# Kernel tuning notes

Hardware: AMD Instinct MI355X
Metric: run time of the kernel (lower is better)

The kernel has to match this reference:

```python
import jax, jax.numpy as jnp
import numpy as np


def setup_inputs() -> dict:
    key = jax.random.key(0)
    k1, k2, k3, k4 = jax.random.split(key, 4)
    T, B, D_in, D_out = 512, 128, 512, 512
    X = jax.random.normal(k1, (T, B, D_in), dtype=jnp.float32)
    # torch nn.Linear default init: U(-1/sqrt(fan_in), 1/sqrt(fan_in))
    lim_in = 1.0 / np.sqrt(D_in)
    lim_h = 1.0 / np.sqrt(D_out)
    W_in = jax.random.uniform(k2, (D_out, D_in), jnp.float32, -lim_in, lim_in)
    W_h = jax.random.uniform(k3, (D_out, D_out), jnp.float32, -lim_h, lim_h)
    b_h = jax.random.uniform(k4, (D_out,), jnp.float32, -lim_h, lim_h)
    return {"X": X, "W_in": W_in, "W_h": W_h, "b_h": b_h}


def reference(X, W_in, W_h, b_h):
    # X: [T, B, D_in]. h_{t+1} = sigmoid(x_t @ W_in^T + h_t @ W_h^T + b_h)
    B = X.shape[1]
    D_out = W_h.shape[0]
    # Precompute all input projections in one big GEMM (same math).
    Xproj = jnp.einsum('tbi,oi->tbo', X, W_in)  # [T, B, D_out]
    h0 = jnp.zeros((B, D_out), dtype=X.dtype)

    def step(h, xp):
        h_new = jax.nn.sigmoid(xp + h @ W_h.T + b_h)
        return h_new, None

    h_last, _ = jax.lax.scan(step, h0, Xproj)
    return h_last
```

## Files before the change

kernel.cpp:

```cpp
#include <hip/hip_runtime.h>
#include <hip/hip_bf16.h>
#include <stdint.h>

typedef _Float16 f16;
typedef _Float16 f16x2 __attribute__((ext_vector_type(2)));
typedef _Float16 f16x4 __attribute__((ext_vector_type(4)));
typedef _Float16 f16x8 __attribute__((ext_vector_type(8)));
typedef float f32x4 __attribute__((ext_vector_type(4)));
typedef int   i32x4 __attribute__((ext_vector_type(4)));

#define T_STEPS 512
#define BATCH   128
#define DD      512
#define LOG2E   1.44269504088896f

#define XP_OFF  0
#define WF_OFF  (67108864)
#define WHQ_OFF (67108864 + 524288)
#define SC_OFF  (67108864 + 524288 + 262144)

__device__ __forceinline__ f16x2 pk(float a, float b) {
    return __builtin_bit_cast(f16x2, __builtin_amdgcn_cvt_pkrtz(a, b));
}

__device__ __forceinline__ float fast_exp2(float x) {
#if __has_builtin(__builtin_amdgcn_exp2f)
    return __builtin_amdgcn_exp2f(x);
#else
    return exp2f(x);
#endif
}

__device__ __forceinline__ float fast_rcp(float x) {
#if __has_builtin(__builtin_amdgcn_rcpf)
    return __builtin_amdgcn_rcpf(x);
#else
    return 1.0f / x;
#endif
}

__device__ __forceinline__ uint32_t pack_u8(float s, int pos, uint32_t old) {
#if __has_builtin(__builtin_amdgcn_cvt_pk_u8_f32)
    return __builtin_amdgcn_cvt_pk_u8_f32(s, pos, old);
#else
    return old | (((uint32_t)(int)s & 0xFF) << (8 * pos));
#endif
}

#define GLDS(g, l) __builtin_amdgcn_global_load_lds(                               \
        (const __attribute__((address_space(1))) void*)(g),                        \
        (__attribute__((address_space(3))) void*)(l), 16, 0, 0)

__global__ __launch_bounds__(256) void prep_kernel(
        const float* __restrict__ Win, f16* __restrict__ Wf) {
    int idx = blockIdx.x * 256 + threadIdx.x;
    if (idx < 262144) Wf[idx] = (f16)Win[idx];
}

__global__ __launch_bounds__(64) void quant_kernel(
        const float* __restrict__ Wh, char* __restrict__ Whq, float* __restrict__ scales) {
    const int o = blockIdx.x, t = threadIdx.x;
    const float* row = Wh + (size_t)o * 512;
    float v[8];
    float m = 0.f;
#pragma unroll
    for (int j = 0; j < 8; j++) { v[j] = row[t * 8 + j]; m = fmaxf(m, fabsf(v[j])); }
#pragma unroll
    for (int off = 32; off > 0; off >>= 1) m = fmaxf(m, __shfl_xor(m, off));
    if (t == 0) scales[o] = -LOG2E * m * (1.0f / (127.0f * 127.0f));
    const float inv = 127.0f / m;
    const int rt = o >> 4, rl = o & 15;
    const int k0 = t * 8;
    const int ks = k0 >> 6, qq = (k0 >> 4) & 3, j0 = k0 & 15;
    const int l = qq * 16 + rl;
    char* dst = Whq + ((size_t)((rt * 8 + ks) * 64 + l)) * 16 + j0;
#pragma unroll
    for (int j = 0; j < 8; j++) dst[j] = (char)rintf(v[j] * inv);
}

__global__ __launch_bounds__(512, 2) void gemm_kernel(
        const float* __restrict__ X, const f16* __restrict__ Wf,
        const float* __restrict__ bias, f16* __restrict__ Xp) {
    const int tid = threadIdx.x;
    const int l = tid & 63, w = tid >> 6;
    const int q = l >> 4, rl = l & 15;
    const int wm = w >> 2, wn = w & 3;
    const int blk = blockIdx.x;
    const int xcd = blk & 7, idx = blk >> 3;
    const int m_blk = (xcd * 64 + (idx >> 1)) * 128;
    const int n_blk = (idx & 1) * 256;

    __shared__ __align__(16) float As[3][128 * 32];
    __shared__ __align__(16) f16   Bs[3][256 * 32];

    const float* aSrc[2];
#pragma unroll
    for (int c = 0; c < 2; c++)
        aSrc[c] = X + (size_t)(m_blk + w * 16 + c * 8 + (l >> 3)) * 512
                    + (((l & 7) ^ (l >> 3)) << 2);
    const f16* bSrc[2];
#pragma unroll
    for (int c = 0; c < 2; c++)
        bSrc[c] = Wf + (size_t)(n_blk + c * 128 + w * 16 + (l >> 2)) * 512
                     + (((l & 3) ^ ((l >> 3) & 3)) << 3);

#define STAGE(kt, sel) do {                                                        \
        const int kf_ = (kt) * 32;                                                 \
        GLDS(aSrc[0] + kf_, &As[sel][(w * 16 + 0) * 32]);                          \
        GLDS(aSrc[1] + kf_, &As[sel][(w * 16 + 8) * 32]);                          \
        GLDS(bSrc[0] + kf_, &Bs[sel][(0 * 128 + w * 16) * 32]);                    \
        GLDS(bSrc[1] + kf_, &Bs[sel][(1 * 128 + w * 16) * 32]);                    \
    } while (0)

    f32x4 acc[4][4] = {};
    const int swA0 = (((2 * q)     ^ (rl & 7)) << 2);
    const int swA1 = (((2 * q + 1) ^ (rl & 7)) << 2);
    const int swB  = ((q ^ ((rl >> 1) & 3)) << 3);

    STAGE(0, 0);
    STAGE(1, 1);

#pragma unroll
    for (int t = 0; t < 16; ++t) {
        const int cur = t % 3;
        if (t < 15) asm volatile("s_waitcnt vmcnt(4)" ::: "memory");
        else        asm volatile("s_waitcnt vmcnt(0)" ::: "memory");
        __builtin_amdgcn_s_barrier();
        if (t + 2 < 16) STAGE(t + 2, (t + 2) % 3);

        f16x8 af4[4], bf4[4];
#pragma unroll
        for (int i = 0; i < 4; i++) {
            const int row = wm * 64 + i * 16 + rl;
            const float4 h0 = *(const float4*)&As[cur][row * 32 + swA0];
            const float4 h1 = *(const float4*)&As[cur][row * 32 + swA1];
            f16x2 p0 = pk(h0.x, h0.y), p1 = pk(h0.z, h0.w);
            f16x2 p2 = pk(h1.x, h1.y), p3 = pk(h1.z, h1.w);
            f16x8 tv;
            tv[0] = p0[0]; tv[1] = p0[1]; tv[2] = p1[0]; tv[3] = p1[1];
            tv[4] = p2[0]; tv[5] = p2[1]; tv[6] = p3[0]; tv[7] = p3[1];
            af4[i] = tv;
        }
#pragma unroll
        for (int j = 0; j < 4; j++) {
            const int row = wn * 64 + j * 16 + rl;
            bf4[j] = *(const f16x8*)&Bs[cur][row * 32 + swB];
        }
#pragma unroll
        for (int i = 0; i < 4; i++)
#pragma unroll
            for (int j = 0; j < 4; j++)
                acc[i][j] = __builtin_amdgcn_mfma_f32_16x16x32_f16(bf4[j], af4[i], acc[i][j], 0, 0, 0);
    }
#undef STAGE
#pragma unroll
    for (int j = 0; j < 4; j++) {
        const float4 b4 = *(const float4*)&bias[n_blk + wn * 64 + j * 16 + q * 4];
        const float bb[4] = {b4.x, b4.y, b4.z, b4.w};
#pragma unroll
        for (int i = 0; i < 4; i++) {
            const int m = m_blk + wm * 64 + i * 16 + rl;
            f16x4 v;
#pragma unroll
            for (int r = 0; r < 4; r++)
                v[r] = (f16)(-LOG2E * (acc[i][j][r] + bb[r]));
            *(f16x4*)(Xp + (size_t)m * 512 + n_blk + wn * 64 + j * 16 + q * 4) = v;
        }
    }
}

__global__ __launch_bounds__(1024) void rnn_kernel(
        const char* __restrict__ Whq, const float* __restrict__ scales,
        const f16* __restrict__ Xp, float* __restrict__ out) {
    const int wg = blockIdx.x;
    const int tid = threadIdx.x;
    const int l = tid & 63, w = tid >> 6;
    const int bl = l & 15;
    const int q = l >> 4;
    const int b = wg * 16 + bl;

    __shared__ __align__(16) uint32_t hT[2][2048];

    i32x4 af[2][8];
    {
        const i32x4* wp = (const i32x4*)Whq;
#pragma unroll
        for (int mt = 0; mt < 2; mt++)
#pragma unroll
            for (int ks = 0; ks < 8; ks++)
                af[mt][ks] = wp[((w * 2 + mt) * 8 + ks) * 64 + l];
    }
    float sc[2][4];
#pragma unroll
    for (int mt = 0; mt < 2; mt++)
#pragma unroll
        for (int r = 0; r < 4; r++)
            sc[mt][r] = scales[w * 32 + mt * 16 + q * 4 + r];

    for (int i = tid; i < 2048; i += 1024) hT[0][i] = 0u;
    __syncthreads();

    const f16* xpb = Xp + (size_t)b * 512 + w * 32 + q * 4;
    f16x4 xn0 = *(const f16x4*)(xpb);
    f16x4 xn1 = *(const f16x4*)(xpb + 16);

    const float K127 = 1.0f / 127.0f;
    for (int t = 0; t < T_STEPS; t++) {
        f16x4 xc0 = xn0, xc1 = xn1;
        const size_t tn = (size_t)(t < T_STEPS - 1 ? t + 1 : t) * (BATCH * 512);
        xn0 = *(const f16x4*)(xpb + tn);
        xn1 = *(const f16x4*)(xpb + tn + 16);

        const int rb = t & 1;
        i32x4 acc[2] = {};
        const uint32_t* hrow = &hT[rb][l * 4];
#pragma unroll
        for (int ks = 0; ks < 8; ks++) {
            i32x4 bfr = *(const i32x4*)(hrow + ks * 256);
            acc[0] = __builtin_amdgcn_mfma_i32_16x16x64_i8(af[0][ks], bfr, acc[0], 0, 0, 0);
            acc[1] = __builtin_amdgcn_mfma_i32_16x16x64_i8(af[1][ks], bfr, acc[1], 0, 0, 0);
        }
#pragma unroll
        for (int mt = 0; mt < 2; mt++) {
            uint32_t pkq = 0;
#pragma unroll
            for (int r = 0; r < 4; r++) {
                float tt = fmaf((float)acc[mt][r], sc[mt][r], (float)(mt == 0 ? xc0[r] : xc1[r]));
                float e  = fast_exp2(tt);
                float eq = fmaf(e, K127, K127);
                float sg = fast_rcp(eq) + 0.5f;
                pkq = pack_u8(sg, r, pkq);
            }
            hT[1 - rb][(w * 2 + mt) * 64 + bl * 4 + q] = pkq;
        }
        __syncthreads();
    }
#pragma unroll
    for (int mt = 0; mt < 2; mt++) {
        uint32_t pkq = hT[T_STEPS & 1][(w * 2 + mt) * 64 + bl * 4 + q];
        float4 o;
        o.x = (float)((pkq      ) & 0xFF) * K127;
        o.y = (float)((pkq >>  8) & 0xFF) * K127;
        o.z = (float)((pkq >> 16) & 0xFF) * K127;
        o.w = (float)((pkq >> 24) & 0xFF) * K127;
        *(float4*)(out + (size_t)b * 512 + w * 32 + mt * 16 + q * 4) = o;
    }
}

extern "C" void kernel_launch(void* const* d_in, const int* in_sizes, int n_in,
                              void* d_out, int out_size, void* d_ws, size_t ws_size,
                              hipStream_t stream) {
    const float* X   = (const float*)d_in[0];
    const float* Win = (const float*)d_in[1];
    const float* Wh  = (const float*)d_in[2];
    const float* bh  = (const float*)d_in[3];
    float* out = (float*)d_out;
    char* ws = (char*)d_ws;
    f16* Xp      = (f16*)(ws + XP_OFF);
    f16* Wf      = (f16*)(ws + WF_OFF);
    char* Whq    = (char*)(ws + WHQ_OFF);
    float* Sc    = (float*)(ws + SC_OFF);

    prep_kernel<<<1024, 256, 0, stream>>>(Win, Wf);
    quant_kernel<<<512, 64, 0, stream>>>(Wh, Whq, Sc);
    gemm_kernel<<<1024, 512, 0, stream>>>(X, Wf, bh, Xp);
    rnn_kernel<<<8, 1024, 0, stream>>>(Whq, Sc, Xp, out);
}
```

Before: 700.9 us.

## Pre-convert X to fp16 and use double-buffered f16 GEMM path

Adds a separate kernel that converts X from fp32 to fp16 into workspace, plus a GEMM variant that loads fp16 A tiles directly and drops the per-tile in-register conversion. The fallback fp32 GEMM moves from triple to double buffering with __syncthreads in place of explicit waitcnt. The new path adds a full read of X and a write of 64MB of fp16, which is extra memory traffic compared with the single fused pass. It is used only when the workspace is large enough.

Measured after the change: 705.2 us. About the same (+0.6%).

```diff
diff --git a/kernel.cpp b/kernel.cpp
--- a/kernel.cpp
+++ b/kernel.cpp
@@ -18,6 +18,8 @@
 #define WF_OFF  (67108864)
 #define WHQ_OFF (67108864 + 524288)
 #define SC_OFF  (67108864 + 524288 + 262144)
+#define XF_OFF  (67108864 + 524288 + 262144 + 2048)
+#define WS_NEED ((size_t)XF_OFF + 67108864)
 
 __device__ __forceinline__ f16x2 pk(float a, float b) {
     return __builtin_bit_cast(f16x2, __builtin_amdgcn_cvt_pkrtz(a, b));
@@ -55,6 +57,17 @@
         const float* __restrict__ Win, f16* __restrict__ Wf) {
     int idx = blockIdx.x * 256 + threadIdx.x;
     if (idx < 262144) Wf[idx] = (f16)Win[idx];
+}
+
+__global__ __launch_bounds__(256) void xcvt_kernel(
+        const float* __restrict__ X, f16* __restrict__ Xf) {
+    const float4* src = (const float4*)X;
+    for (int k = blockIdx.x * 256 + threadIdx.x; k < 8388608; k += 8192 * 256) {
+        float4 v = src[k];
+        f16x4 o;
+        o[0] = (f16)v.x; o[1] = (f16)v.y; o[2] = (f16)v.z; o[3] = (f16)v.w;
+        *(f16x4*)(Xf + (size_t)k * 4) = o;
+    }
 }
 
 __global__ __launch_bounds__(64) void quant_kernel(
@@ -78,7 +91,79 @@
     for (int j = 0; j < 8; j++) dst[j] = (char)rintf(v[j] * inv);
 }
 
-__global__ __launch_bounds__(512, 2) void gemm_kernel(
+__global__ __launch_bounds__(512, 2) void gemm_f16_kernel(
+        const f16* __restrict__ Xf, const f16* __restrict__ Wf,
+        const float* __restrict__ bias, f16* __restrict__ Xp) {
+    const int tid = threadIdx.x;
+    const int l = tid & 63, w = tid >> 6;
+    const int q = l >> 4, rl = l & 15;
+    const int wm = w >> 2, wn = w & 3;
+    const int blk = blockIdx.x;
+    const int xcd = blk & 7, idx = blk >> 3;
+    const int m_blk = (xcd * 64 + (idx >> 1)) * 128;
+    const int n_blk = (idx & 1) * 256;
+
+    __shared__ __align__(16) f16 As[2][128 * 32];
+    __shared__ __align__(16) f16 Bs[2][256 * 32];
+
+    const f16* aSrc = Xf + (size_t)(m_blk + w * 16 + (l >> 2)) * 512
+                         + (((l & 3) ^ ((l >> 3) & 3)) << 3);
+    const f16* bSrc[2];
+#pragma unroll
+    for (int c = 0; c < 2; c++)
+        bSrc[c] = Wf + (size_t)(n_blk + c * 128 + w * 16 + (l >> 2)) * 512
+                     + (((l & 3) ^ ((l >> 3) & 3)) << 3);
+
+    f32x4 acc[4][4] = {};
+    const int swf = ((q ^ ((rl >> 1) & 3)) << 3);
+
+    GLDS(aSrc, &As[0][(w * 16) * 32]);
+#pragma unroll
+    for (int c = 0; c < 2; c++) GLDS(bSrc[c], &Bs[0][(c * 128 + w * 16) * 32]);
+
+    for (int t = 0; t < 16; ++t) {
+        const int cur = t & 1;
+        __syncthreads();
+        if (t < 15) {
+            const int kf = (t + 1) * 32;
+            GLDS(aSrc + kf, &As[cur ^ 1][(w * 16) * 32]);
+#pragma unroll
+            for (int c = 0; c < 2; c++) GLDS(bSrc[c] + kf, &Bs[cur ^ 1][(c * 128 + w * 16) * 32]);
+        }
+        f16x8 af4[4], bf4[4];
+#pragma unroll
+        for (int i = 0; i < 4; i++) {
+            const int row = wm * 64 + i * 16 + rl;
+            af4[i] = *(const f16x8*)&As[cur][row * 32 + swf];
+        }
+#pragma unroll
+        for (int j = 0; j < 4; j++) {
+            const int row = wn * 64 + j * 16 + rl;
+            bf4[j] = *(const f16x8*)&Bs[cur][row * 32 + swf];
+        }
+#pragma unroll
+        for (int i = 0; i < 4; i++)
+#pragma unroll
+            for (int j = 0; j < 4; j++)
+                acc[i][j] = __builtin_amdgcn_mfma_f32_16x16x32_f16(bf4[j], af4[i], acc[i][j], 0, 0, 0);
+    }
+#pragma unroll
+    for (int j = 0; j < 4; j++) {
+        const float4 b4 = *(const float4*)&bias[n_blk + wn * 64 + j * 16 + q * 4];
+        const float bb[4] = {b4.x, b4.y, b4.z, b4.w};
+#pragma unroll
+        for (int i = 0; i < 4; i++) {
+            const int m = m_blk + wm * 64 + i * 16 + rl;
+            f16x4 v;
+#pragma unroll
+            for (int r = 0; r < 4; r++)
+                v[r] = (f16)(-LOG2E * (acc[i][j][r] + bb[r]));
+            *(f16x4*)(Xp + (size_t)m * 512 + n_blk + wn * 64 + j * 16 + q * 4) = v;
+        }
+    }
+}
+
+__global__ __launch_bounds__(512, 2) void gemm_f32_kernel(
         const float* __restrict__ X, const f16* __restrict__ Wf,
         const float* __restrict__ bias, f16* __restrict__ Xp) {
     const int tid = threadIdx.x;
@@ -90,8 +175,8 @@
     const int m_blk = (xcd * 64 + (idx >> 1)) * 128;
     const int n_blk = (idx & 1) * 256;
 
-    __shared__ __align__(16) float As[3][128 * 32];
-    __shared__ __align__(16) f16   Bs[3][256 * 32];
+    __shared__ __align__(16) float As[2][128 * 32];
+    __shared__ __align__(16) f16   Bs[2][256 * 32];
 
     const float* aSrc[2];
 #pragma unroll
@@ -104,30 +189,26 @@
         bSrc[c] = Wf + (size_t)(n_blk + c * 128 + w * 16 + (l >> 2)) * 512
                      + (((l & 3) ^ ((l >> 3) & 3)) << 3);
 
-#define STAGE(kt, sel) do {                                                        \
-        const int kf_ = (kt) * 32;                                                 \
-        GLDS(aSrc[0] + kf_, &As[sel][(w * 16 + 0) * 32]);                          \
-        GLDS(aSrc[1] + kf_, &As[sel][(w * 16 + 8) * 32]);                          \
-        GLDS(bSrc[0] + kf_, &Bs[sel][(0 * 128 + w * 16) * 32]);                    \
-        GLDS(bSrc[1] + kf_, &Bs[sel][(1 * 128 + w * 16) * 32]);                    \
-    } while (0)
-
     f32x4 acc[4][4] = {};
     const int swA0 = (((2 * q)     ^ (rl & 7)) << 2);
     const int swA1 = (((2 * q + 1) ^ (rl & 7)) << 2);
     const int swB  = ((q ^ ((rl >> 1) & 3)) << 3);
 
-    STAGE(0, 0);
-    STAGE(1, 1);
-
-#pragma unroll
+#pragma unroll
+    for (int c = 0; c < 2; c++) GLDS(aSrc[c], &As[0][(w * 16 + c * 8) * 32]);
+#pragma unroll
+    for (int c = 0; c < 2; c++) GLDS(bSrc[c], &Bs[0][(c * 128 + w * 16) * 32]);
+
     for (int t = 0; t < 16; ++t) {
-        const int cur = t % 3;
-        if (t < 15) asm volatile("s_waitcnt vmcnt(4)" ::: "memory");
-        else        asm volatile("s_waitcnt vmcnt(0)" ::: "memory");
-        __builtin_amdgcn_s_barrier();
-        if (t + 2 < 16) STAGE(t + 2, (t + 2) % 3);
-
+        const int cur = t & 1;
+        __syncthreads();
+        if (t < 15) {
+            const int kf = (t + 1) * 32;
+#pragma unroll
+            for (int c = 0; c < 2; c++) GLDS(aSrc[c] + kf, &As[cur ^ 1][(w * 16 + c * 8) * 32]);
+#pragma unroll
+            for (int c = 0; c < 2; c++) GLDS(bSrc[c] + kf, &Bs[cur ^ 1][(c * 128 + w * 16) * 32]);
+        }
         f16x8 af4[4], bf4[4];
 #pragma unroll
         for (int i = 0; i < 4; i++) {
@@ -152,7 +233,6 @@
             for (int j = 0; j < 4; j++)
                 acc[i][j] = __builtin_amdgcn_mfma_f32_16x16x32_f16(bf4[j], af4[i], acc[i][j], 0, 0, 0);
     }
-#undef STAGE
 #pragma unroll
     for (int j = 0; j < 4; j++) {
         const float4 b4 = *(const float4*)&bias[n_blk + wn * 64 + j * 16 + q * 4];
@@ -260,9 +340,15 @@
     f16* Wf      = (f16*)(ws + WF_OFF);
     char* Whq    = (char*)(ws + WHQ_OFF);
     float* Sc    = (float*)(ws + SC_OFF);
+    f16* Xf      = (f16*)(ws + XF_OFF);
 
     prep_kernel<<<1024, 256, 0, stream>>>(Win, Wf);
     quant_kernel<<<512, 64, 0, stream>>>(Wh, Whq, Sc);
-    gemm_kernel<<<1024, 512, 0, stream>>>(X, Wf, bh, Xp);
+    if (ws_size >= WS_NEED) {
+        xcvt_kernel<<<8192, 256, 0, stream>>>(X, Xf);
+        gemm_f16_kernel<<<1024, 512, 0, stream>>>(Xf, Wf, bh, Xp);
+    } else {
+        gemm_f32_kernel<<<1024, 512, 0, stream>>>(X, Wf, bh, Xp);
+    }
     rnn_kernel<<<8, 1024, 0, stream>>>(Whq, Sc, Xp, out);
 }
```

## Fuse input-projection GEMM and RNN recurrence into one kernel with per-timestep flags

Applied to the files above, without the earlier changes.

Merges the GEMM and the recurrent kernel into one launch. Blocks 0-7 run the serial recurrence while the remaining blocks compute the input projection per timestep panel and publish completion through atomic counters, so the recurrence can start before the whole GEMM is done. The GEMM tiles shrink to 128x256 with 1024 threads and double buffering instead of triple buffering. It relies on the RNN blocks being resident while they spin-wait on counters. The counter polling and sleeps add latency inside the serial loop, and the GEMM is reshaped in a way that may lower its throughput.

Result: slower. 1.393 ms (+98.8%).

```diff
diff --git a/kernel.cpp b/kernel.cpp
--- a/kernel.cpp
+++ b/kernel.cpp
@@ -18,6 +18,7 @@
 #define WF_OFF  (67108864)
 #define WHQ_OFF (67108864 + 524288)
 #define SC_OFF  (67108864 + 524288 + 262144)
+#define CNT_OFF (SC_OFF + 2048)
 
 __device__ __forceinline__ f16x2 pk(float a, float b) {
     return __builtin_bit_cast(f16x2, __builtin_amdgcn_cvt_pkrtz(a, b));
@@ -52,9 +53,10 @@
         (__attribute__((address_space(3))) void*)(l), 16, 0, 0)
 
 __global__ __launch_bounds__(256) void prep_kernel(
-        const float* __restrict__ Win, f16* __restrict__ Wf) {
+        const float* __restrict__ Win, f16* __restrict__ Wf, int* __restrict__ cnt) {
     int idx = blockIdx.x * 256 + threadIdx.x;
     if (idx < 262144) Wf[idx] = (f16)Win[idx];
+    if (idx < 512) cnt[idx] = 0;
 }
 
 __global__ __launch_bounds__(64) void quant_kernel(
@@ -78,109 +80,98 @@
     for (int j = 0; j < 8; j++) dst[j] = (char)rintf(v[j] * inv);
 }
 
-__global__ __launch_bounds__(512, 2) void gemm_kernel(
+__global__ __launch_bounds__(1024, 4) void fused_kernel(
         const float* __restrict__ X, const f16* __restrict__ Wf,
-        const float* __restrict__ bias, f16* __restrict__ Xp) {
+        const float* __restrict__ bias, f16* __restrict__ Xp,
+        const char* __restrict__ Whq, const float* __restrict__ scales,
+        int* __restrict__ cnt, float* __restrict__ out) {
+    __shared__ __align__(16) char smem[65536];
     const int tid = threadIdx.x;
     const int l = tid & 63, w = tid >> 6;
-    const int q = l >> 4, rl = l & 15;
-    const int wm = w >> 2, wn = w & 3;
-    const int blk = blockIdx.x;
-    const int xcd = blk & 7, idx = blk >> 3;
-    const int m_blk = (xcd * 64 + (idx >> 1)) * 128;
-    const int n_blk = (idx & 1) * 256;
-
-    __shared__ __align__(16) float As[3][128 * 32];
-    __shared__ __align__(16) f16   Bs[3][256 * 32];
-
-    const float* aSrc[2];
-#pragma unroll
-    for (int c = 0; c < 2; c++)
-        aSrc[c] = X + (size_t)(m_blk + w * 16 + c * 8 + (l >> 3)) * 512
-                    + (((l & 7) ^ (l >> 3)) << 2);
-    const f16* bSrc[2];
-#pragma unroll
-    for (int c = 0; c < 2; c++)
-        bSrc[c] = Wf + (size_t)(n_blk + c * 128 + w * 16 + (l >> 2)) * 512
-                     + (((l & 3) ^ ((l >> 3) & 3)) << 3);
-
-#define STAGE(kt, sel) do {                                                        \
-        const int kf_ = (kt) * 32;                                                 \
-        GLDS(aSrc[0] + kf_, &As[sel][(w * 16 + 0) * 32]);                          \
-        GLDS(aSrc[1] + kf_, &As[sel][(w * 16 + 8) * 32]);                          \
-        GLDS(bSrc[0] + kf_, &Bs[sel][(0 * 128 + w * 16) * 32]);                    \
-        GLDS(bSrc[1] + kf_, &Bs[sel][(1 * 128 + w * 16) * 32]);                    \
-    } while (0)
-
-    f32x4 acc[4][4] = {};
-    const int swA0 = (((2 * q)     ^ (rl & 7)) << 2);
-    const int swA1 = (((2 * q + 1) ^ (rl & 7)) << 2);
-    const int swB  = ((q ^ ((rl >> 1) & 3)) << 3);
-
-    STAGE(0, 0);
-    STAGE(1, 1);
-
-#pragma unroll
-    for (int t = 0; t < 16; ++t) {
-        const int cur = t % 3;
-        if (t < 15) asm volatile("s_waitcnt vmcnt(4)" ::: "memory");
-        else        asm volatile("s_waitcnt vmcnt(0)" ::: "memory");
-        __builtin_amdgcn_s_barrier();
-        if (t + 2 < 16) STAGE(t + 2, (t + 2) % 3);
-
-        f16x8 af4[4], bf4[4];
-#pragma unroll
-        for (int i = 0; i < 4; i++) {
-            const int row = wm * 64 + i * 16 + rl;
-            const float4 h0 = *(const float4*)&As[cur][row * 32 + swA0];
-            const float4 h1 = *(const float4*)&As[cur][row * 32 + swA1];
-            f16x2 p0 = pk(h0.x, h0.y), p1 = pk(h0.z, h0.w);
-            f16x2 p2 = pk(h1.x, h1.y), p3 = pk(h1.z, h1.w);
-            f16x8 tv;
-            tv[0] = p0[0]; tv[1] = p0[1]; tv[2] = p1[0]; tv[3] = p1[1];
-            tv[4] = p2[0]; tv[5] = p2[1]; tv[6] = p3[0]; tv[7] = p3[1];
-            af4[i] = tv;
+
+    if (blockIdx.x >= 8) {
+        float (*As)[128 * 32] = (float (*)[128 * 32])smem;
+        f16   (*Bs)[256 * 32] = (f16 (*)[256 * 32])(smem + 32768);
+        const int b0 = (int)blockIdx.x - 8;
+        const int panel = ((b0 >> 4) << 3) | (b0 & 7);
+        const int half  = (b0 >> 3) & 1;
+        const int m_blk = panel * 128;
+        const int n_blk = half * 256;
+        const int q = l >> 4, rl = l & 15;
+        const int wm = w >> 2, wn = w & 3;
+
+        const float* aSrc = X + (size_t)(m_blk + w * 8 + (l >> 3)) * 512
+                              + (((l & 7) ^ (l >> 3)) << 2);
+        const f16* bSrc = Wf + (size_t)(n_blk + w * 16 + (l >> 2)) * 512
+                             + (((l & 3) ^ ((l >> 3) & 3)) << 3);
+
+        f32x4 acc[2][4] = {};
+        const int swA0 = (((2 * q)     ^ (rl & 7)) << 2);
+        const int swA1 = (((2 * q + 1) ^ (rl & 7)) << 2);
+        const int swB  = ((q ^ ((rl >> 1) & 3)) << 3);
+
+        GLDS(aSrc, &As[0][(w * 8) * 32]);
+        GLDS(bSrc, &Bs[0][(w * 16) * 32]);
+
+        for (int t = 0; t < 16; ++t) {
+            const int cur = t & 1;
+            __syncthreads();
+            if (t < 15) {
+                const int kf = (t + 1) * 32;
+                GLDS(aSrc + kf, &As[cur ^ 1][(w * 8) * 32]);
+                GLDS(bSrc + kf, &Bs[cur ^ 1][(w * 16) * 32]);
+            }
+            f16x8 af4[2], bf4[4];
+#pragma unroll
+            for (int i = 0; i < 2; i++) {
+                const int row = wm * 32 + i * 16 + rl;
+                const float4 h0 = *(const float4*)&As[cur][row * 32 + swA0];
+                const float4 h1 = *(const float4*)&As[cur][row * 32 + swA1];
+                f16x2 p0 = pk(h0.x, h0.y), p1 = pk(h0.z, h0.w);
+                f16x2 p2 = pk(h1.x, h1.y), p3 = pk(h1.z, h1.w);
+                f16x8 tv;
+                tv[0] = p0[0]; tv[1] = p0[1]; tv[2] = p1[0]; tv[3] = p1[1];
+                tv[4] = p2[0]; tv[5] = p2[1]; tv[6] = p3[0]; tv[7] = p3[1];
+                af4[i] = tv;
+            }
+#pragma unroll
+            for (int j = 0; j < 4; j++) {
+                const int row = wn * 64 + j * 16 + rl;
+                bf4[j] = *(const f16x8*)&Bs[cur][row * 32 + swB];
+            }
+#pragma unroll
+            for (int i = 0; i < 2; i++)
+#pragma unroll
+                for (int j = 0; j < 4; j++)
+                    acc[i][j] = __builtin_amdgcn_mfma_f32_16x16x32_f16(bf4[j], af4[i], acc[i][j], 0, 0, 0);
         }
 #pragma unroll
         for (int j = 0; j < 4; j++) {
-            const int row = wn * 64 + j * 16 + rl;
-            bf4[j] = *(const f16x8*)&Bs[cur][row * 32 + swB];
-        }
-#pragma unroll
-        for (int i = 0; i < 4; i++)
-#pragma unroll
-            for (int j = 0; j < 4; j++)
-                acc[i][j] = __builtin_amdgcn_mfma_f32_16x16x32_f16(bf4[j], af4[i], acc[i][j], 0, 0, 0);
-    }
-#undef STAGE
-#pragma unroll
-    for (int j = 0; j < 4; j++) {
-        const float4 b4 = *(const float4*)&bias[n_blk + wn * 64 + j * 16 + q * 4];
-        const float bb[4] = {b4.x, b4.y, b4.z, b4.w};
-#pragma unroll
-        for (int i = 0; i < 4; i++) {
-            const int m = m_blk + wm * 64 + i * 16 + rl;
-            f16x4 v;
-#pragma unroll
-            for (int r = 0; r < 4; r++)
-                v[r] = (f16)(-LOG2E * (acc[i][j][r] + bb[r]));
-            *(f16x4*)(Xp + (size_t)m * 512 + n_blk + wn * 64 + j * 16 + q * 4) = v;
-        }
-    }
-}
-
-__global__ __launch_bounds__(1024) void rnn_kernel(
-        const char* __restrict__ Whq, const float* __restrict__ scales,
-        const f16* __restrict__ Xp, float* __restrict__ out) {
+            const float4 b4 = *(const float4*)&bias[n_blk + wn * 64 + j * 16 + q * 4];
+            const float bb[4] = {b4.x, b4.y, b4.z, b4.w};
+#pragma unroll
+            for (int i = 0; i < 2; i++) {
+                const int m = m_blk + wm * 32 + i * 16 + rl;
+                f16x4 v;
+#pragma unroll
+                for (int r = 0; r < 4; r++)
+                    v[r] = (f16)(-LOG2E * (acc[i][j][r] + bb[r]));
+                *(f16x4*)(Xp + (size_t)m * 512 + n_blk + wn * 64 + j * 16 + q * 4) = v;
+            }
+        }
+        __threadfence();
+        __syncthreads();
+        if (tid == 0)
+            __hip_atomic_fetch_add(cnt + panel, 1, __ATOMIC_RELEASE, __HIP_MEMORY_SCOPE_AGENT);
+        return;
+    }
+
+    uint32_t* hT = (uint32_t*)smem;
     const int wg = blockIdx.x;
-    const int tid = threadIdx.x;
-    const int l = tid & 63, w = tid >> 6;
     const int bl = l & 15;
     const int q = l >> 4;
     const int b = wg * 16 + bl;
 
-    __shared__ __align__(16) uint32_t hT[2][2048];
-
     i32x4 af[2][8];
     {
         const i32x4* wp = (const i32x4*)Whq;
@@ -197,23 +188,40 @@
         for (int r = 0; r < 4; r++)
             sc[mt][r] = scales[w * 32 + mt * 16 + q * 4 + r];
 
-    for (int i = tid; i < 2048; i += 1024) hT[0][i] = 0u;
+    for (int i = tid; i < 2048; i += 1024) hT[i] = 0u;
     __syncthreads();
 
+    int wmk = 0;
+#define ENSURE(n) do {                                                                     \
+        while (wmk <= (n)) {                                                               \
+            const int idx_ = wmk + l;                                                      \
+            int v_ = (idx_ < 512)                                                          \
+                ? __hip_atomic_load(cnt + idx_, __ATOMIC_ACQUIRE, __HIP_MEMORY_SCOPE_AGENT)\
+                : 2;                                                                       \
+            unsigned long long m_ = __ballot(v_ >= 2);                                     \
+            unsigned long long inv_ = ~m_;                                                 \
+            int pre_ = inv_ ? (int)__builtin_ctzll(inv_) : 64;                             \
+            if (pre_ == 0) __builtin_amdgcn_s_sleep(32);                                   \
+            wmk += pre_;                                                                   \
+        }                                                                                  \
+    } while (0)
+
     const f16* xpb = Xp + (size_t)b * 512 + w * 32 + q * 4;
+    ENSURE(0);
     f16x4 xn0 = *(const f16x4*)(xpb);
     f16x4 xn1 = *(const f16x4*)(xpb + 16);
 
     const float K127 = 1.0f / 127.0f;
     for (int t = 0; t < T_STEPS; t++) {
         f16x4 xc0 = xn0, xc1 = xn1;
+        if (t < T_STEPS - 1) ENSURE(t + 1);
         const size_t tn = (size_t)(t < T_STEPS - 1 ? t + 1 : t) * (BATCH * 512);
         xn0 = *(const f16x4*)(xpb + tn);
         xn1 = *(const f16x4*)(xpb + tn + 16);
 
         const int rb = t & 1;
         i32x4 acc[2] = {};
-        const uint32_t* hrow = &hT[rb][l * 4];
+        const uint32_t* hrow = hT + rb * 2048 + l * 4;
 #pragma unroll
         for (int ks = 0; ks < 8; ks++) {
             i32x4 bfr = *(const i32x4*)(hrow + ks * 256);
@@ -231,13 +239,14 @@
                 float sg = fast_rcp(eq) + 0.5f;
                 pkq = pack_u8(sg, r, pkq);
             }
-            hT[1 - rb][(w * 2 + mt) * 64 + bl * 4 + q] = pkq;
+            hT[(1 - rb) * 2048 + (w * 2 + mt) * 64 + bl * 4 + q] = pkq;
         }
         __syncthreads();
     }
+#undef ENSURE
 #pragma unroll
     for (int mt = 0; mt < 2; mt++) {
-        uint32_t pkq = hT[T_STEPS & 1][(w * 2 + mt) * 64 + bl * 4 + q];
+        uint32_t pkq = hT[(T_STEPS & 1) * 2048 + (w * 2 + mt) * 64 + bl * 4 + q];
         float4 o;
         o.x = (float)((pkq      ) & 0xFF) * K127;
         o.y = (float)((pkq >>  8) & 0xFF) * K127;
@@ -260,9 +269,9 @@
     f16* Wf      = (f16*)(ws + WF_OFF);
     char* Whq    = (char*)(ws + WHQ_OFF);
     float* Sc    = (float*)(ws + SC_OFF);
-
-    prep_kernel<<<1024, 256, 0, stream>>>(Win, Wf);
+    int* Cnt     = (int*)(ws + CNT_OFF);
+
+    prep_kernel<<<1024, 256, 0, stream>>>(Win, Wf, Cnt);
     quant_kernel<<<512, 64, 0, stream>>>(Wh, Whq, Sc);
-    gemm_kernel<<<1024, 512, 0, stream>>>(X, Wf, bh, Xp);
-    rnn_kernel<<<8, 1024, 0, stream>>>(Whq, Sc, Xp, out);
-}
+    fused_kernel<<<1032, 1024, 0, stream>>>(X, Wf, bh, Xp, Whq, Sc, Cnt, out);
+}
```
